# Performance work log

Hardware: AMD Instinct MI355X
Metric: run time of the kernel (lower is better)

## Reference

```python
import jax, jax.numpy as jnp
import numpy as np

N = 100000
E = 1000000
D = 64


def setup_inputs() -> dict:
    key = jax.random.key(0)
    k1, k2, k3 = jax.random.split(key, 3)
    x = jax.random.normal(k1, (N, D), dtype=jnp.float32)
    edge_index = jax.random.randint(k2, (2, E), 0, N, dtype=jnp.int64)
    W = jax.random.normal(k3, (D, D), dtype=jnp.float32) * (1.0 / np.sqrt(D))  # nn.Linear weight [out, in]
    return {"x": x, "edge_index": edge_index, "W": W, "num_nodes": N}


def reference(x, edge_index, W, num_nodes):
    src, dst = edge_index[0], edge_index[1]
    # in-degree (counted on dst) + self loop
    deg = jnp.zeros((num_nodes,), dtype=x.dtype).at[dst].add(1.0) + 1.0
    dis = deg ** -0.5  # deg^{-1/2}, shape [N]
    # gather src features, scale by deg_inv_sqrt[src], scatter-add to dst
    msg = x[src] * dis[src][:, None]  # [E, D]
    agg = jnp.zeros_like(x).at[dst].add(msg)  # [N, D]
    # self-loop contribution, then scale by deg_inv_sqrt on the node axis
    agg = (agg + x * dis[:, None]) * dis[:, None]
    # linear (no bias): agg @ W^T with W of shape [out, in]
    return agg @ W.T
```

## Files before the change

### kernel.cpp

```cpp
#include <hip/hip_runtime.h>

#define FD 64

typedef __attribute__((ext_vector_type(8))) short bf16x8;
typedef __attribute__((ext_vector_type(4))) float f32x4;

__device__ inline short f2bf(float f) {
    union { float f; unsigned u; } v; v.f = f;
    unsigned r = (v.u + 0x7fffu + ((v.u >> 16) & 1u)) >> 16;
    return (short)r;
}
__device__ inline float bf2f(unsigned short u) {
    union { unsigned u; float f; } v; v.u = ((unsigned)u) << 16;
    return v.f;
}

__global__ void degpos_kernel(const int* __restrict__ dst, int* __restrict__ degi,
                              unsigned short* __restrict__ pos, int E) {
    int i = blockIdx.x * blockDim.x + threadIdx.x;
    int stride = gridDim.x * blockDim.x;
    for (; i < E; i += stride) {
        pos[i] = (unsigned short)atomicAdd(&degi[dst[i]], 1);
    }
}

#define SCAN_ELEMS 2048

__global__ void scan1_kernel(const int* __restrict__ degi, int* __restrict__ offs,
                             int* __restrict__ bsums, float* __restrict__ dis, int N) {
    __shared__ int tsum[256];
    int base = blockIdx.x * SCAN_ELEMS + threadIdx.x * 8;
    int v[8];
    int s = 0;
    #pragma unroll
    for (int k = 0; k < 8; ++k) {
        int idx = base + k;
        v[k] = (idx < N) ? degi[idx] : 0;
        if (idx < N) dis[idx] = rsqrtf((float)v[k] + 1.0f);
        s += v[k];
    }
    tsum[threadIdx.x] = s;
    __syncthreads();
    for (int off = 1; off < 256; off <<= 1) {
        int t = (threadIdx.x >= off) ? tsum[threadIdx.x - off] : 0;
        __syncthreads();
        tsum[threadIdx.x] += t;
        __syncthreads();
    }
    int excl = (threadIdx.x == 0) ? 0 : tsum[threadIdx.x - 1];
    #pragma unroll
    for (int k = 0; k < 8; ++k) {
        int idx = base + k;
        if (idx < N) offs[idx] = excl;
        excl += v[k];
    }
    if (threadIdx.x == 255) bsums[blockIdx.x] = tsum[255];
}

__global__ void scan2_kernel(int* __restrict__ bsums, int nb) {
    __shared__ int t[256];
    int v = (threadIdx.x < nb) ? bsums[threadIdx.x] : 0;
    t[threadIdx.x] = v;
    __syncthreads();
    for (int off = 1; off < 256; off <<= 1) {
        int u = (threadIdx.x >= off) ? t[threadIdx.x - off] : 0;
        __syncthreads();
        t[threadIdx.x] += u;
        __syncthreads();
    }
    if (threadIdx.x < nb) bsums[threadIdx.x] = (threadIdx.x == 0) ? 0 : t[threadIdx.x - 1];
}

__global__ void scan3_kernel(int* __restrict__ offs, const int* __restrict__ bsums, int N) {
    int i = blockIdx.x * blockDim.x + threadIdx.x;
    if (i < N) offs[i] += bsums[i / SCAN_ELEMS];
}

__global__ void fill_pos_kernel(const int* __restrict__ src, const int* __restrict__ dst,
                                const int* __restrict__ offs, const int* __restrict__ bsums,
                                const unsigned short* __restrict__ pos,
                                int* __restrict__ bucket, int E) {
    int i = blockIdx.x * blockDim.x + threadIdx.x;
    int stride = gridDim.x * blockDim.x;
    for (; i < E; i += stride) {
        int d = dst[i];
        bucket[offs[d] + bsums[d >> 11] + (int)pos[i]] = src[i];
    }
}

__global__ __launch_bounds__(256) void z_mfma_kernel(
        const float* __restrict__ x, const float* __restrict__ dis,
        const float* __restrict__ W, unsigned short* __restrict__ z, int N) {
    int lane = threadIdx.x & 63;
    int r16  = lane & 15;
    int kg   = lane >> 4;

    bf16x8 bfrag[4][2];
    #pragma unroll
    for (int ct = 0; ct < 4; ++ct) {
        #pragma unroll
        for (int kk = 0; kk < 2; ++kk) {
            const float* wp = W + (size_t)(ct * 16 + r16) * FD + kk * 32 + kg * 8;
            float4 w0 = *(const float4*)wp;
            float4 w1 = *(const float4*)(wp + 4);
            bf16x8 b;
            b[0] = f2bf(w0.x); b[1] = f2bf(w0.y); b[2] = f2bf(w0.z); b[3] = f2bf(w0.w);
            b[4] = f2bf(w1.x); b[5] = f2bf(w1.y); b[6] = f2bf(w1.z); b[7] = f2bf(w1.w);
            bfrag[ct][kk] = b;
        }
    }

    int wid    = blockIdx.x * (blockDim.x >> 6) + (threadIdx.x >> 6);
    int nwaves = gridDim.x * (blockDim.x >> 6);
    int tiles  = (N + 15) >> 4;

    for (int t = wid; t < tiles; t += nwaves) {
        int n0  = t << 4;
        int row = n0 + r16;
        int rl  = row < N ? row : N - 1;
        const float* xp = x + (size_t)rl * FD + kg * 8;
        float4 a00 = *(const float4*)(xp);
        float4 a01 = *(const float4*)(xp + 4);
        float4 a10 = *(const float4*)(xp + 32);
        float4 a11 = *(const float4*)(xp + 36);
        bf16x8 a0, a1;
        a0[0] = f2bf(a00.x); a0[1] = f2bf(a00.y); a0[2] = f2bf(a00.z); a0[3] = f2bf(a00.w);
        a0[4] = f2bf(a01.x); a0[5] = f2bf(a01.y); a0[6] = f2bf(a01.z); a0[7] = f2bf(a01.w);
        a1[0] = f2bf(a10.x); a1[1] = f2bf(a10.y); a1[2] = f2bf(a10.z); a1[3] = f2bf(a10.w);
        a1[4] = f2bf(a11.x); a1[5] = f2bf(a11.y); a1[6] = f2bf(a11.z); a1[7] = f2bf(a11.w);

        f32x4 acc[4];
        #pragma unroll
        for (int ct = 0; ct < 4; ++ct) {
            acc[ct] = (f32x4){0.f, 0.f, 0.f, 0.f};
            acc[ct] = __builtin_amdgcn_mfma_f32_16x16x32_bf16(a0, bfrag[ct][0], acc[ct], 0, 0, 0);
            acc[ct] = __builtin_amdgcn_mfma_f32_16x16x32_bf16(a1, bfrag[ct][1], acc[ct], 0, 0, 0);
        }

        #pragma unroll
        for (int reg = 0; reg < 4; ++reg) {
            int nr = n0 + kg * 4 + reg;
            if (nr < N) {
                float dn = dis[nr];
                #pragma unroll
                for (int ct = 0; ct < 4; ++ct) {
                    z[(size_t)nr * FD + ct * 16 + r16] =
                        (unsigned short)f2bf(acc[ct][reg] * dn);
                }
            }
        }
    }
}

__global__ __launch_bounds__(256) void gather_z_kernel(
        const unsigned short* __restrict__ z, const int* __restrict__ offs,
        const int* __restrict__ bsums, const int* __restrict__ degi,
        const int* __restrict__ bucket, const float* __restrict__ dis,
        float* __restrict__ out, int N) {
    int wave = threadIdx.x >> 6;
    int lane = threadIdx.x & 63;
    int n = blockIdx.x * 4 + wave;
    if (n >= N) return;

    const unsigned short* zl = z + lane;
    int j   = offs[n] + bsums[n >> 11];
    int end = j + degi[n];
    float acc = 0.0f;
    for (; j + 7 < end; j += 8) {
        int s0 = bucket[j],     s1 = bucket[j + 1], s2 = bucket[j + 2], s3 = bucket[j + 3];
        int s4 = bucket[j + 4], s5 = bucket[j + 5], s6 = bucket[j + 6], s7 = bucket[j + 7];
        float v0 = bf2f(zl[(size_t)s0 * FD]);
        float v1 = bf2f(zl[(size_t)s1 * FD]);
        float v2 = bf2f(zl[(size_t)s2 * FD]);
        float v3 = bf2f(zl[(size_t)s3 * FD]);
        float v4 = bf2f(zl[(size_t)s4 * FD]);
        float v5 = bf2f(zl[(size_t)s5 * FD]);
        float v6 = bf2f(zl[(size_t)s6 * FD]);
        float v7 = bf2f(zl[(size_t)s7 * FD]);
        acc += ((v0 + v1) + (v2 + v3)) + ((v4 + v5) + (v6 + v7));
    }
    for (; j + 3 < end; j += 4) {
        int s0 = bucket[j], s1 = bucket[j + 1], s2 = bucket[j + 2], s3 = bucket[j + 3];
        float v0 = bf2f(zl[(size_t)s0 * FD]);
        float v1 = bf2f(zl[(size_t)s1 * FD]);
        float v2 = bf2f(zl[(size_t)s2 * FD]);
        float v3 = bf2f(zl[(size_t)s3 * FD]);
        acc += (v0 + v1) + (v2 + v3);
    }
    for (; j < end; ++j) {
        acc += bf2f(zl[(size_t)bucket[j] * FD]);
    }
    out[(size_t)n * FD + lane] = (acc + bf2f(zl[(size_t)n * FD])) * dis[n];
}

__global__ void deg_kernel(const int* __restrict__ dst, int* __restrict__ degi, int E) {
    int i = blockIdx.x * blockDim.x + threadIdx.x;
    int stride = gridDim.x * blockDim.x;
    for (; i < E; i += stride) {
        atomicAdd(&degi[dst[i]], 1);
    }
}

__global__ void fill_kernel(const int* __restrict__ src, const int* __restrict__ dst,
                            const int* __restrict__ offs, int* __restrict__ cursor,
                            int* __restrict__ bucket, int E) {
    int i = blockIdx.x * blockDim.x + threadIdx.x;
    int stride = gridDim.x * blockDim.x;
    for (; i < E; i += stride) {
        int d = dst[i];
        int p = atomicAdd(&cursor[d], 1);
        bucket[offs[d] + p] = src[i];
    }
}

__global__ __launch_bounds__(256) void gather_linear_kernel(
        const float* __restrict__ x, const int* __restrict__ offs,
        const int* __restrict__ degi, const int* __restrict__ bucket,
        const float* __restrict__ dis, const float* __restrict__ W,
        float* __restrict__ out, int N) {
    __shared__ float Wt[FD][FD + 1];
    __shared__ float rows[4][FD];

    for (int t = threadIdx.x; t < FD * FD; t += 256) {
        Wt[t & 63][t >> 6] = W[t];
    }
    __syncthreads();

    int wave = threadIdx.x >> 6;
    int lane = threadIdx.x & 63;
    int n = blockIdx.x * 4 + wave;

    if (n < N) {
        int j   = offs[n];
        int end = j + degi[n];
        float acc = 0.0f;
        for (; j + 3 < end; j += 4) {
            int s0 = bucket[j], s1 = bucket[j + 1], s2 = bucket[j + 2], s3 = bucket[j + 3];
            float d0 = dis[s0], d1 = dis[s1], d2 = dis[s2], d3 = dis[s3];
            float v0 = x[(size_t)s0 * FD + lane];
            float v1 = x[(size_t)s1 * FD + lane];
            float v2 = x[(size_t)s2 * FD + lane];
            float v3 = x[(size_t)s3 * FD + lane];
            acc += v0 * d0 + v1 * d1 + v2 * d2 + v3 * d3;
        }
        for (; j < end; ++j) {
            int s = bucket[j];
            acc += x[(size_t)s * FD + lane] * dis[s];
        }
        float dn = dis[n];
        rows[wave][lane] = (acc + x[(size_t)n * FD + lane] * dn) * dn;
    }
    if (n < N) {
        float o = 0.0f;
        #pragma unroll
        for (int i = 0; i < FD; i += 4) {
            float4 r = *(const float4*)&rows[wave][i];
            o += r.x * Wt[i + 0][lane]
               + r.y * Wt[i + 1][lane]
               + r.z * Wt[i + 2][lane]
               + r.w * Wt[i + 3][lane];
        }
        out[(size_t)n * FD + lane] = o;
    }
}

extern "C" void kernel_launch(void* const* d_in, const int* in_sizes, int n_in,
                              void* d_out, int out_size, void* d_ws, size_t ws_size,
                              hipStream_t stream) {
    const float* x  = (const float*)d_in[0];
    const int*   ei = (const int*)d_in[1];
    const float* W  = (const float*)d_in[2];

    const int N = in_sizes[0] / FD;
    const int E = in_sizes[1] / 2;
    const int* src = ei;
    const int* dst = ei + E;

    float* out = (float*)d_out;
    const int nb = (N + SCAN_ELEMS - 1) / SCAN_ELEMS;

    size_t posB = (((size_t)E * 2) + 3) & ~(size_t)3;
    size_t need_full = ((size_t)N * 3 + 1024 + (size_t)E) * 4 + posB + (size_t)N * FD * 2;

    if (ws_size >= need_full) {
        char* ws = (char*)d_ws;
        int*   degi   = (int*)ws;    ws += (size_t)N * 4;
        float* dis    = (float*)ws;  ws += (size_t)N * 4;
        int*   offs   = (int*)ws;    ws += (size_t)N * 4;
        int*   bsums  = (int*)ws;    ws += 1024 * 4;
        int*   bucket = (int*)ws;    ws += (size_t)E * 4;
        unsigned short* pos = (unsigned short*)ws;  ws += posB;
        unsigned short* z   = (unsigned short*)ws;

        hipMemsetAsync(degi, 0, (size_t)N * 4, stream);
        degpos_kernel<<<2048, 256, 0, stream>>>(dst, degi, pos, E);
        scan1_kernel<<<nb, 256, 0, stream>>>(degi, offs, bsums, dis, N);
        scan2_kernel<<<1, 256, 0, stream>>>(bsums, nb);
        z_mfma_kernel<<<512, 256, 0, stream>>>(x, dis, W, z, N);
        fill_pos_kernel<<<2048, 256, 0, stream>>>(src, dst, offs, bsums, pos, bucket, E);
        gather_z_kernel<<<(N + 3) / 4, 256, 0, stream>>>(z, offs, bsums, degi, bucket, dis, out, N);
    } else {
        char* ws = (char*)d_ws;
        int*   degi   = (int*)ws;    ws += (size_t)N * 4;
        float* dis    = (float*)ws;  ws += (size_t)N * 4;
        int*   offs   = (int*)ws;    ws += (size_t)N * 4;
        int*   cursor = (int*)ws;    ws += (size_t)N * 4;
        int*   bsums  = (int*)ws;    ws += 1024 * 4;
        int*   bucket = (int*)ws;

        hipMemsetAsync(degi,   0, (size_t)N * 4, stream);
        hipMemsetAsync(cursor, 0, (size_t)N * 4, stream);
        deg_kernel<<<2048, 256, 0, stream>>>(dst, degi, E);
        scan1_kernel<<<nb, 256, 0, stream>>>(degi, offs, bsums, dis, N);
        scan2_kernel<<<1, 256, 0, stream>>>(bsums, nb);
        scan3_kernel<<<(N + 255) / 256, 256, 0, stream>>>(offs, bsums, N);
        fill_kernel<<<2048, 256, 0, stream>>>(src, dst, offs, cursor, bucket, E);
        gather_linear_kernel<<<(N + 3) / 4, 256, 0, stream>>>(
            x, offs, degi, bucket, dis, W, out, N);
    }
}
```

Measured before the change: 134.8 us.

## Replace per-edge position array with cursor atomics and vectorize edge loops

Drops the 16-bit per-edge position array written by the degree pass. Bucket slots are now claimed with atomic cursors, initialised from the scanned offsets by a new small kernel, and the degree and fill passes read src/dst as int4 vectors. The gather kernel becomes grid-stride with a fixed block count, and the z_mfma grid is doubled. This removes the pos write and read traffic but adds a second round of atomics in the fill pass plus an extra kernel launch. It also makes edge order within each bucket nondeterministic.

```diff
diff --git a/kernel.cpp b/kernel.cpp
--- a/kernel.cpp
+++ b/kernel.cpp
@@ -15,12 +15,19 @@
     return v.f;
 }
 
-__global__ void degpos_kernel(const int* __restrict__ dst, int* __restrict__ degi,
-                              unsigned short* __restrict__ pos, int E) {
+__global__ void deg_hist_kernel(const int* __restrict__ dst, int* __restrict__ degi, int E) {
     int i = blockIdx.x * blockDim.x + threadIdx.x;
     int stride = gridDim.x * blockDim.x;
-    for (; i < E; i += stride) {
-        pos[i] = (unsigned short)atomicAdd(&degi[dst[i]], 1);
+    int e4 = E >> 2;
+    for (int k = i; k < e4; k += stride) {
+        int4 d = ((const int4*)dst)[k];
+        atomicAdd(&degi[d.x], 1);
+        atomicAdd(&degi[d.y], 1);
+        atomicAdd(&degi[d.z], 1);
+        atomicAdd(&degi[d.w], 1);
+    }
+    if (i < (E & 3)) {
+        atomicAdd(&degi[dst[(e4 << 2) + i]], 1);
     }
 }
 
@@ -76,15 +83,28 @@
     if (i < N) offs[i] += bsums[i / SCAN_ELEMS];
 }
 
-__global__ void fill_pos_kernel(const int* __restrict__ src, const int* __restrict__ dst,
-                                const int* __restrict__ offs, const int* __restrict__ bsums,
-                                const unsigned short* __restrict__ pos,
-                                int* __restrict__ bucket, int E) {
+__global__ void cursor_init_kernel(const int* __restrict__ offs, const int* __restrict__ bsums,
+                                   int* __restrict__ cursor, int N) {
+    int i = blockIdx.x * blockDim.x + threadIdx.x;
+    if (i < N) cursor[i] = offs[i] + bsums[i >> 11];
+}
+
+__global__ void fill_cur_kernel(const int* __restrict__ src, const int* __restrict__ dst,
+                                int* __restrict__ cursor, int* __restrict__ bucket, int E) {
     int i = blockIdx.x * blockDim.x + threadIdx.x;
     int stride = gridDim.x * blockDim.x;
-    for (; i < E; i += stride) {
-        int d = dst[i];
-        bucket[offs[d] + bsums[d >> 11] + (int)pos[i]] = src[i];
+    int e4 = E >> 2;
+    for (int k = i; k < e4; k += stride) {
+        int4 d = ((const int4*)dst)[k];
+        int4 s = ((const int4*)src)[k];
+        bucket[atomicAdd(&cursor[d.x], 1)] = s.x;
+        bucket[atomicAdd(&cursor[d.y], 1)] = s.y;
+        bucket[atomicAdd(&cursor[d.z], 1)] = s.z;
+        bucket[atomicAdd(&cursor[d.w], 1)] = s.w;
+    }
+    if (i < (E & 3)) {
+        int e = (e4 << 2) + i;
+        bucket[atomicAdd(&cursor[dst[e]], 1)] = src[e];
     }
 }
 
@@ -152,45 +172,49 @@
     }
 }
 
+#define GATHER_BLOCKS 2048
+
 __global__ __launch_bounds__(256) void gather_z_kernel(
         const unsigned short* __restrict__ z, const int* __restrict__ offs,
         const int* __restrict__ bsums, const int* __restrict__ degi,
         const int* __restrict__ bucket, const float* __restrict__ dis,
         float* __restrict__ out, int N) {
-    int wave = threadIdx.x >> 6;
     int lane = threadIdx.x & 63;
-    int n = blockIdx.x * 4 + wave;
-    if (n >= N) return;
+    int wid  = (blockIdx.x * blockDim.x + threadIdx.x) >> 6;
+    int nw   = (gridDim.x * blockDim.x) >> 6;
 
     const unsigned short* zl = z + lane;
-    int j   = offs[n] + bsums[n >> 11];
-    int end = j + degi[n];
-    float acc = 0.0f;
-    for (; j + 7 < end; j += 8) {
-        int s0 = bucket[j],     s1 = bucket[j + 1], s2 = bucket[j + 2], s3 = bucket[j + 3];
-        int s4 = bucket[j + 4], s5 = bucket[j + 5], s6 = bucket[j + 6], s7 = bucket[j + 7];
-        float v0 = bf2f(zl[(size_t)s0 * FD]);
-        float v1 = bf2f(zl[(size_t)s1 * FD]);
-        float v2 = bf2f(zl[(size_t)s2 * FD]);
-        float v3 = bf2f(zl[(size_t)s3 * FD]);
-        float v4 = bf2f(zl[(size_t)s4 * FD]);
-        float v5 = bf2f(zl[(size_t)s5 * FD]);
-        float v6 = bf2f(zl[(size_t)s6 * FD]);
-        float v7 = bf2f(zl[(size_t)s7 * FD]);
-        acc += ((v0 + v1) + (v2 + v3)) + ((v4 + v5) + (v6 + v7));
-    }
-    for (; j + 3 < end; j += 4) {
-        int s0 = bucket[j], s1 = bucket[j + 1], s2 = bucket[j + 2], s3 = bucket[j + 3];
-        float v0 = bf2f(zl[(size_t)s0 * FD]);
-        float v1 = bf2f(zl[(size_t)s1 * FD]);
-        float v2 = bf2f(zl[(size_t)s2 * FD]);
-        float v3 = bf2f(zl[(size_t)s3 * FD]);
-        acc += (v0 + v1) + (v2 + v3);
-    }
-    for (; j < end; ++j) {
-        acc += bf2f(zl[(size_t)bucket[j] * FD]);
-    }
-    out[(size_t)n * FD + lane] = (acc + bf2f(zl[(size_t)n * FD])) * dis[n];
+
+    for (int n = wid; n < N; n += nw) {
+        int j   = offs[n] + bsums[n >> 11];
+        int end = j + degi[n];
+        float acc = 0.0f;
+        for (; j + 7 < end; j += 8) {
+            int s0 = bucket[j],     s1 = bucket[j + 1], s2 = bucket[j + 2], s3 = bucket[j + 3];
+            int s4 = bucket[j + 4], s5 = bucket[j + 5], s6 = bucket[j + 6], s7 = bucket[j + 7];
+            float v0 = bf2f(zl[(size_t)s0 * FD]);
+            float v1 = bf2f(zl[(size_t)s1 * FD]);
+            float v2 = bf2f(zl[(size_t)s2 * FD]);
+            float v3 = bf2f(zl[(size_t)s3 * FD]);
+            float v4 = bf2f(zl[(size_t)s4 * FD]);
+            float v5 = bf2f(zl[(size_t)s5 * FD]);
+            float v6 = bf2f(zl[(size_t)s6 * FD]);
+            float v7 = bf2f(zl[(size_t)s7 * FD]);
+            acc += ((v0 + v1) + (v2 + v3)) + ((v4 + v5) + (v6 + v7));
+        }
+        for (; j + 3 < end; j += 4) {
+            int s0 = bucket[j], s1 = bucket[j + 1], s2 = bucket[j + 2], s3 = bucket[j + 3];
+            float v0 = bf2f(zl[(size_t)s0 * FD]);
+            float v1 = bf2f(zl[(size_t)s1 * FD]);
+            float v2 = bf2f(zl[(size_t)s2 * FD]);
+            float v3 = bf2f(zl[(size_t)s3 * FD]);
+            acc += (v0 + v1) + (v2 + v3);
+        }
+        for (; j < end; ++j) {
+            acc += bf2f(zl[(size_t)bucket[j] * FD]);
+        }
+        out[(size_t)n * FD + lane] = (acc + bf2f(zl[(size_t)n * FD])) * dis[n];
+    }
 }
 
 __global__ void deg_kernel(const int* __restrict__ dst, int* __restrict__ degi, int E) {
@@ -279,26 +303,27 @@
     float* out = (float*)d_out;
     const int nb = (N + SCAN_ELEMS - 1) / SCAN_ELEMS;
 
-    size_t posB = (((size_t)E * 2) + 3) & ~(size_t)3;
-    size_t need_full = ((size_t)N * 3 + 1024 + (size_t)E) * 4 + posB + (size_t)N * FD * 2;
+    size_t need_full = ((size_t)N * 4 + 1024 + (size_t)E) * 4 + (size_t)N * FD * 2;
 
     if (ws_size >= need_full) {
         char* ws = (char*)d_ws;
         int*   degi   = (int*)ws;    ws += (size_t)N * 4;
         float* dis    = (float*)ws;  ws += (size_t)N * 4;
         int*   offs   = (int*)ws;    ws += (size_t)N * 4;
+        int*   cursor = (int*)ws;    ws += (size_t)N * 4;
         int*   bsums  = (int*)ws;    ws += 1024 * 4;
         int*   bucket = (int*)ws;    ws += (size_t)E * 4;
-        unsigned short* pos = (unsigned short*)ws;  ws += posB;
-        unsigned short* z   = (unsigned short*)ws;
+        unsigned short* z = (unsigned short*)ws;
 
         hipMemsetAsync(degi, 0, (size_t)N * 4, stream);
-        degpos_kernel<<<2048, 256, 0, stream>>>(dst, degi, pos, E);
+        deg_hist_kernel<<<1024, 256, 0, stream>>>(dst, degi, E);
         scan1_kernel<<<nb, 256, 0, stream>>>(degi, offs, bsums, dis, N);
         scan2_kernel<<<1, 256, 0, stream>>>(bsums, nb);
-        z_mfma_kernel<<<512, 256, 0, stream>>>(x, dis, W, z, N);
-        fill_pos_kernel<<<2048, 256, 0, stream>>>(src, dst, offs, bsums, pos, bucket, E);
-        gather_z_kernel<<<(N + 3) / 4, 256, 0, stream>>>(z, offs, bsums, degi, bucket, dis, out, N);
+        cursor_init_kernel<<<(N + 255) / 256, 256, 0, stream>>>(offs, bsums, cursor, N);
+        z_mfma_kernel<<<1024, 256, 0, stream>>>(x, dis, W, z, N);
+        fill_cur_kernel<<<1024, 256, 0, stream>>>(src, dst, cursor, bucket, E);
+        gather_z_kernel<<<GATHER_BLOCKS, 256, 0, stream>>>(
+            z, offs, bsums, degi, bucket, dis, out, N);
     } else {
         char* ws = (char*)d_ws;
         int*   degi   = (int*)ws;    ws += (size_t)N * 4;
```

After: 182.6 us. 1.35x slower.
